# Kernel optimization log

Measured on AMD Instinct MI355X. Metric: run time of the kernel, lower is better.

## Reference

```python
import jax, jax.numpy as jnp
import numpy as np

IMG_SIZE = 640
STRIDES = (8, 16, 32)
KA = 3          # anchors per level
C = 80          # num classes
CONF_THRESH = 0.001
NMS_THRESH = 0.6
TOPK = 4096     # fixed candidate cap for jit-compatible NMS


def setup_inputs() -> dict:
    key = jax.random.key(0)
    k1, k2, k3 = jax.random.split(key, 3)
    ch = KA * (1 + C + 4)  # 255
    pred_s = jax.random.normal(k1, (ch, 80, 80), dtype=jnp.float32)
    pred_m = jax.random.normal(k2, (ch, 40, 40), dtype=jnp.float32)
    pred_l = jax.random.normal(k3, (ch, 20, 20), dtype=jnp.float32)
    # classic YOLOv3 anchors, [level, anchor, (w,h)]
    anchor_size = jnp.array(
        [[[10, 13], [16, 30], [33, 23]],
         [[30, 61], [62, 45], [59, 119]],
         [[116, 90], [156, 198], [373, 326]]], dtype=jnp.float32)
    return {"pred_s": pred_s, "pred_m": pred_m, "pred_l": pred_l,
            "anchor_size": anchor_size}


def _decode_level(pred, anchors, stride):
    # pred: [KA*(1+C+4), H, W]; anchors: [KA, 2]
    H, W = pred.shape[1], pred.shape[2]
    p = jnp.transpose(pred, (1, 2, 0))                    # [H, W, ch]
    obj = p[..., :KA].reshape(-1, 1)                      # [H*W*KA, 1]
    cls = p[..., KA:KA * (1 + C)].reshape(-1, C)          # [H*W*KA, C]
    reg = p[..., KA * (1 + C):].reshape(H * W, KA, 4)     # [H*W, KA, 4]
    gy, gx = jnp.meshgrid(jnp.arange(H), jnp.arange(W), indexing="ij")
    grid = jnp.stack([gx, gy], -1).reshape(-1, 1, 2).astype(pred.dtype)  # [H*W,1,2]
    # center_sample = False branch
    xy = (jax.nn.sigmoid(reg[..., :2]) + grid) * stride
    wh = jnp.exp(reg[..., 2:]) * anchors[None, :, :]
    box = jnp.concatenate([xy - 0.5 * wh, xy + 0.5 * wh], -1).reshape(-1, 4)
    return obj, cls, box


def _decode(pred_s, pred_m, pred_l, anchor_size):
    parts = [_decode_level(p, anchor_size[i], STRIDES[i])
             for i, p in enumerate([pred_s, pred_m, pred_l])]
    obj = jnp.concatenate([p[0] for p in parts], 0)       # [N,1]
    cls = jnp.concatenate([p[1] for p in parts], 0)       # [N,C]
    box = jnp.concatenate([p[2] for p in parts], 0)       # [N,4]
    bboxes = jnp.clip(box / IMG_SIZE, 0.0, 1.0)
    scores = jax.nn.sigmoid(obj) * jax.nn.softmax(cls, axis=-1)
    return bboxes, scores


def reference(pred_s, pred_m, pred_l, anchor_size):
    bboxes, scores = _decode(pred_s, pred_m, pred_l, anchor_size)
    cls_inds = jnp.argmax(scores, axis=1)                 # [N]
    sc = jnp.max(scores, axis=1)                          # [N]
    sc_masked = jnp.where(sc >= CONF_THRESH, sc, -1.0)
    top_sc, idx = jax.lax.top_k(sc_masked, TOPK)          # candidates, score-sorted
    b = bboxes[idx]                                       # [K,4]
    c = cls_inds[idx]                                     # [K]
    valid = top_sc >= CONF_THRESH                         # [K]
    # pairwise IoU, exactly as the numpy NMS computes it
    x1, y1, x2, y2 = b[:, 0], b[:, 1], b[:, 2], b[:, 3]
    area = (x2 - x1) * (y2 - y1)
    xx1 = jnp.maximum(x1[:, None], x1[None, :])
    yy1 = jnp.maximum(y1[:, None], y1[None, :])
    xx2 = jnp.minimum(x2[:, None], x2[None, :])
    yy2 = jnp.minimum(y2[:, None], y2[None, :])
    w = jnp.maximum(1e-28, xx2 - xx1)
    h = jnp.maximum(1e-28, yy2 - yy1)
    inter = w * h
    iou = inter / (area[:, None] + area[None, :] - inter + 1e-14)
    # sup[j, i] = kept j (earlier in score order) suppresses i, same class only
    order = jnp.arange(TOPK)
    sup = (c[:, None] == c[None, :]) & (iou > NMS_THRESH) \
          & (order[:, None] < order[None, :])
    def body(i, keep):
        ki = valid[i] & ~jnp.any(keep & sup[:, i])
        return keep.at[i].set(ki)
    keep = jax.lax.fori_loop(0, TOPK, body, jnp.zeros(TOPK, dtype=bool))
    return b, top_sc, c, keep
```

## Files before the change

### kernel.cpp

```cpp
#include <hip/hip_runtime.h>
#include <cstdint>
#include <cstddef>

#define N_ANCH 25200
#define NB0 19200
#define NB1 24000
#define TOPK_N 4096
#define CONF_T 0.001
#define NMS_T 0.6
#define IMGS 640.0
#define NBINS 8192
#define JS 16

typedef unsigned long long u64;

struct WS {
  alignas(64) double sc[N_ANCH];
  alignas(64) double box[N_ANCH][4];
  alignas(64) int    cls[N_ANCH];
  alignas(64) int    binv[N_ANCH];
  alignas(64) int    rank[N_ANCH];
  alignas(64) int    subset[N_ANCH];
  alignas(64) double ssc[N_ANCH];
  int    m_count;
  int    t_bin;
  alignas(64) double tbox[TOPK_N][4];
  alignas(64) double tarea[TOPK_N];
  alignas(64) double tsc[TOPK_N];
  alignas(64) int    tcls[TOPK_N];
  alignas(64) u64    supT[TOPK_N * 64];
  alignas(64) u64    hasSup[64];
};

__device__ __forceinline__ double dsigmoid(double x) { return 1.0 / (1.0 + exp(-x)); }

__device__ __forceinline__ int score_bin(double sc) {
  if (sc < 0.0) return 0;
  return (int)(__float_as_uint((float)sc) >> 17);
}

__global__ void k_decode(const float* __restrict__ ps, const float* __restrict__ pm,
                         const float* __restrict__ pl, const float* __restrict__ anch,
                         WS* __restrict__ ws) {
  int tid = blockIdx.x * 256 + threadIdx.x;
  int a = tid >> 2;
  int r = tid & 3;
  if (a >= N_ANCH) return;
  const float* p; int W, base, lvl; double stride;
  if (a < NB0)      { p = ps; W = 80; base = 0;   lvl = 0; stride = 8.0; }
  else if (a < NB1) { p = pm; W = 40; base = NB0; lvl = 1; stride = 16.0; }
  else              { p = pl; W = 20; base = NB1; lvl = 2; stride = 32.0; }
  int e = a - base;
  int pos = e / 3;
  int k = e - 3 * pos;
  int HW = W * W;

  const float* pc = p + (size_t)(3 + k * 80) * HW + pos;
  double m = -1e300, ssum = 0.0; int am = 0;
  for (int t = 0; t < 20; ++t) {
    int c = r + 4 * t;
    double v = (double)pc[(size_t)c * HW];
    ssum += exp(v);
    if (v > m) { m = v; am = c; }
  }
  for (int off = 1; off <= 2; off <<= 1) {
    double om = __shfl_xor(m, off);
    int oam   = __shfl_xor(am, off);
    double os = __shfl_xor(ssum, off);
    ssum += os;
    if (om > m || (om == m && oam < am)) { m = om; am = oam; }
  }

  if (r == 0) {
    double sobj = dsigmoid((double)p[(size_t)k * HW + pos]);
    double sc = sobj * (exp(m) / ssum);

    int x = pos % W, y = pos / W;
    const float* pr = p + (size_t)(243 + k * 4) * HW + pos;
    double tx = (double)pr[0];
    double ty = (double)pr[(size_t)HW];
    double tw = (double)pr[(size_t)2 * HW];
    double th = (double)pr[(size_t)3 * HW];
    double cx = (dsigmoid(tx) + (double)x) * stride;
    double cy = (dsigmoid(ty) + (double)y) * stride;
    double aw = (double)anch[lvl * 6 + k * 2 + 0];
    double ah = (double)anch[lvl * 6 + k * 2 + 1];
    double bw = exp(tw) * aw;
    double bh = exp(th) * ah;
    double x1 = fmin(fmax((cx - 0.5 * bw) / IMGS, 0.0), 1.0);
    double y1 = fmin(fmax((cy - 0.5 * bh) / IMGS, 0.0), 1.0);
    double x2 = fmin(fmax((cx + 0.5 * bw) / IMGS, 0.0), 1.0);
    double y2 = fmin(fmax((cy + 0.5 * bh) / IMGS, 0.0), 1.0);

    ws->box[a][0] = x1; ws->box[a][1] = y1;
    ws->box[a][2] = x2; ws->box[a][3] = y2;
    ws->cls[a] = am;
    double scm = (sc >= CONF_T) ? sc : -1.0;
    ws->sc[a] = scm;
    ws->binv[a] = score_bin(scm);
  }
}

__global__ void __launch_bounds__(1024) k_select(WS* __restrict__ ws) {
  __shared__ int hist[NBINS];
  __shared__ int part[1024];
  int t = threadIdx.x;
  for (int i = t; i < NBINS; i += 1024) hist[i] = 0;
  __syncthreads();
  for (int i = t; i < N_ANCH; i += 1024) atomicAdd(&hist[ws->binv[i]], 1);
  __syncthreads();
  const int CH = NBINS / 1024;
  int sum = 0;
  for (int rr = 0; rr < CH; ++rr) sum += hist[NBINS - 1 - (t * CH + rr)];
  part[t] = sum;
  __syncthreads();
  for (int off = 1; off < 1024; off <<= 1) {
    int v = (t >= off) ? part[t - off] : 0;
    __syncthreads();
    part[t] += v;
    __syncthreads();
  }
  int cum = part[t] - sum;
  for (int rr = 0; rr < CH; ++rr) {
    int b = NBINS - 1 - (t * CH + rr);
    int h = hist[b];
    int prev = cum;
    cum += h;
    if (prev < TOPK_N && cum >= TOPK_N) ws->t_bin = b;
  }
  if (t == 0) ws->m_count = 0;
}

__global__ void k_compact(WS* __restrict__ ws) {
  int i = blockIdx.x * 256 + threadIdx.x;
  if (i < 64) ws->hasSup[i] = 0ull;
  if (i >= N_ANCH) return;
  int tb = ws->t_bin;
  if (ws->binv[i] >= tb) {
    int idx = atomicAdd(&ws->m_count, 1);
    ws->subset[idx] = i;
    ws->ssc[idx] = ws->sc[i];
    ws->rank[idx] = 0;
  }
}

__global__ void k_rank(WS* __restrict__ ws) {
  const int CHUNK = 1024;
  __shared__ double sj[CHUNK];
  __shared__ int    aj[CHUNK];
  int m = ws->m_count;
  if ((int)blockIdx.x * 256 >= m) return;
  int i = blockIdx.x * 256 + threadIdx.x;
  bool active = (i < m);
  int ai = active ? ws->subset[i] : 0;
  double si = active ? ws->ssc[i] : -2.0;

  int jlen = (m + JS - 1) / JS;
  int j0 = blockIdx.y * jlen;
  int jend = min(j0 + jlen, m);
  int cnt = 0;
  for (int jc = j0; jc < jend; jc += CHUNK) {
    int n = min(CHUNK, jend - jc);
    __syncthreads();
    for (int t = threadIdx.x; t < n; t += 256) {
      aj[t] = ws->subset[jc + t];
      sj[t] = ws->ssc[jc + t];
    }
    __syncthreads();
    if (active) {
      for (int t = 0; t < n; ++t) {
        double s = sj[t];
        cnt += (int)((s > si) | ((s == si) & (aj[t] < ai)));
      }
    }
  }
  if (active && cnt) atomicAdd(&ws->rank[i], cnt);
}

__global__ void k_scatter(WS* __restrict__ ws, float* __restrict__ out) {
  int m = ws->m_count;
  int i = blockIdx.x * 256 + threadIdx.x;
  if (i >= m) return;
  int r = ws->rank[i];
  if (r >= TOPK_N) return;
  int a = ws->subset[i];
  double b0 = ws->box[a][0], b1 = ws->box[a][1];
  double b2 = ws->box[a][2], b3 = ws->box[a][3];
  double s  = ws->ssc[i];
  int    c  = ws->cls[a];
  ws->tbox[r][0] = b0; ws->tbox[r][1] = b1;
  ws->tbox[r][2] = b2; ws->tbox[r][3] = b3;
  ws->tarea[r] = (b2 - b0) * (b3 - b1);
  ws->tsc[r] = s;
  ws->tcls[r] = c;
  out[r * 4 + 0] = (float)b0;
  out[r * 4 + 1] = (float)b1;
  out[r * 4 + 2] = (float)b2;
  out[r * 4 + 3] = (float)b3;
  out[4 * TOPK_N + r] = (float)s;
  out[5 * TOPK_N + r] = (float)c;
}

__global__ void k_iou(WS* __restrict__ ws) {
  int tid = threadIdx.x;
  int w = blockIdx.y;
  int i0 = blockIdx.x * 256;
  int jbase = w * 64;
  if (jbase >= i0 + 256) {
    ws->supT[(size_t)(i0 + tid) * 64 + w] = 0ull;
    return;
  }
  __shared__ double jb[64][5];
  __shared__ int jc[64];
  if (tid < 64) {
    int j = jbase + tid;
    jb[tid][0] = ws->tbox[j][0];
    jb[tid][1] = ws->tbox[j][1];
    jb[tid][2] = ws->tbox[j][2];
    jb[tid][3] = ws->tbox[j][3];
    jb[tid][4] = ws->tarea[j];
    jc[tid] = ws->tcls[j];
  }
  __syncthreads();
  int i = i0 + tid;
  double x1 = ws->tbox[i][0], y1 = ws->tbox[i][1];
  double x2 = ws->tbox[i][2], y2 = ws->tbox[i][3];
  double ai = ws->tarea[i];
  int ci = ws->tcls[i];
  u64 bits = 0;
  for (int t = 0; t < 64; ++t) {
    double xx1 = fmax(x1, jb[t][0]);
    double yy1 = fmax(y1, jb[t][1]);
    double xx2 = fmin(x2, jb[t][2]);
    double yy2 = fmin(y2, jb[t][3]);
    double iw = fmax(1e-28, xx2 - xx1);
    double ih = fmax(1e-28, yy2 - yy1);
    double inter = iw * ih;
    double denom = ai + jb[t][4] - inter + 1e-14;
    bool sup = (jc[t] == ci) && (inter > NMS_T * denom) && ((jbase + t) < i);
    bits |= ((u64)sup) << t;
  }
  ws->supT[(size_t)i * 64 + w] = bits;
  if (bits) atomicOr(&ws->hasSup[i >> 6], 1ull << (i & 63));
}

__global__ void __launch_bounds__(64) k_nms(const WS* __restrict__ ws, float* __restrict__ out) {
  __shared__ u64 hsArr[64];
  __shared__ int lst[TOPK_N];
  int lane = threadIdx.x;

  u64 validw = 0;
  const double4* tp = (const double4*)(ws->tsc + lane * 64);
  for (int q = 0; q < 16; ++q) {
    double4 v = tp[q];
    validw |= ((u64)(v.x >= CONF_T)) << (q * 4 + 0);
    validw |= ((u64)(v.y >= CONF_T)) << (q * 4 + 1);
    validw |= ((u64)(v.z >= CONF_T)) << (q * 4 + 2);
    validw |= ((u64)(v.w >= CONF_T)) << (q * 4 + 3);
  }

  u64 hasw = ws->hasSup[lane];
  u64 keepw = validw & ~hasw;
  hsArr[lane] = hasw;
  __syncthreads();

  int K = 0;
  for (int l = 0; l < 64; ++l) {
    u64 w = hsArr[l];
    while (w) {
      int b = __builtin_ctzll(w);
      w &= w - 1;
      if (lane == 0) lst[K] = l * 64 + b;
      ++K;
    }
  }
  __syncthreads();

  const u64* ST = ws->supT;
  int IA[16], IB[16];
  u64 A[16], B[16];

#pragma unroll
  for (int r = 0; r < 16; ++r) IA[r] = (r < K) ? lst[r] : 0;
#pragma unroll
  for (int r = 0; r < 16; ++r) A[r] = (r < K) ? ST[(size_t)IA[r] * 64 + lane] : 0ull;

  for (int base = 0; base < K; base += 32) {
#pragma unroll
    for (int r = 0; r < 16; ++r) IB[r] = (base + 16 + r < K) ? lst[base + 16 + r] : 0;
#pragma unroll
    for (int r = 0; r < 16; ++r) B[r] = (base + 16 + r < K) ? ST[(size_t)IB[r] * 64 + lane] : 0ull;
#pragma unroll
    for (int r = 0; r < 16; ++r) {
      if (base + r < K) {
        int i = IA[r];
        u64 bal = __ballot((keepw & A[r]) != 0ull);
        if (lane == (i >> 6) && bal == 0ull && ((validw >> (i & 63)) & 1ull))
          keepw |= 1ull << (i & 63);
      }
    }
#pragma unroll
    for (int r = 0; r < 16; ++r) IA[r] = (base + 32 + r < K) ? lst[base + 32 + r] : 0;
#pragma unroll
    for (int r = 0; r < 16; ++r) A[r] = (base + 32 + r < K) ? ST[(size_t)IA[r] * 64 + lane] : 0ull;
#pragma unroll
    for (int r = 0; r < 16; ++r) {
      if (base + 16 + r < K) {
        int i = IB[r];
        u64 bal = __ballot((keepw & B[r]) != 0ull);
        if (lane == (i >> 6) && bal == 0ull && ((validw >> (i & 63)) & 1ull))
          keepw |= 1ull << (i & 63);
      }
    }
  }

  for (int b = 0; b < 64; ++b)
    out[6 * TOPK_N + lane * 64 + b] = (float)((keepw >> b) & 1ull);
}

extern "C" void kernel_launch(void* const* d_in, const int* in_sizes, int n_in,
                              void* d_out, int out_size, void* d_ws, size_t ws_size,
                              hipStream_t stream) {
  const float* ps   = (const float*)d_in[0];
  const float* pm   = (const float*)d_in[1];
  const float* pl   = (const float*)d_in[2];
  const float* anch = (const float*)d_in[3];
  float* out = (float*)d_out;
  WS* ws = (WS*)d_ws;

  dim3 blk(256);
  k_decode <<<dim3((N_ANCH * 4 + 255) / 256), blk, 0, stream>>>(ps, pm, pl, anch, ws);
  k_select <<<dim3(1), dim3(1024), 0, stream>>>(ws);
  k_compact<<<dim3((N_ANCH + 255) / 256), blk, 0, stream>>>(ws);
  k_rank   <<<dim3((N_ANCH + 255) / 256, JS), blk, 0, stream>>>(ws);
  k_scatter<<<dim3((N_ANCH + 255) / 256), blk, 0, stream>>>(ws, out);
  k_iou    <<<dim3(TOPK_N / 256, 64), blk, 0, stream>>>(ws);
  k_nms    <<<dim3(1), dim3(64), 0, stream>>>(ws, out);
}
```

Measured before the change: 124.1 us.

## Fuse all NMS pipeline stages into one cooperative kernel with grid syncs

The seven separate launches (decode, select, compact, rank, scatter, IoU, NMS) are replaced by one cooperative kernel of 256 blocks × 512 threads, with grid.sync between stages. This removes per-launch overhead and gaps between kernels. The score histogram is now built with global atomics during decode instead of in a single-block pass. Compaction uses wave-aggregated atomics, and rank and IoU work is spread over persistent blocks through task loops. In exchange it adds grid-wide barrier costs, global-atomic contention on the histogram, and leaves most of the grid idle during the single-block select and NMS stages.

```diff
diff --git a/kernel.cpp b/kernel.cpp
--- a/kernel.cpp
+++ b/kernel.cpp
@@ -1,6 +1,9 @@
 #include <hip/hip_runtime.h>
+#include <hip/hip_cooperative_groups.h>
 #include <cstdint>
 #include <cstddef>
+
+namespace cg = cooperative_groups;
 
 #define N_ANCH 25200
 #define NB0 19200
@@ -10,7 +13,9 @@
 #define NMS_T 0.6
 #define IMGS 640.0
 #define NBINS 8192
-#define JS 16
+#define JS 32
+#define NBLK 256
+#define NTHR 512
 
 typedef unsigned long long u64;
 
@@ -22,6 +27,8 @@
   alignas(64) int    rank[N_ANCH];
   alignas(64) int    subset[N_ANCH];
   alignas(64) double ssc[N_ANCH];
+  alignas(64) int    hist[NBINS];
+  alignas(64) u64    hasSup[64];
   int    m_count;
   int    t_bin;
   alignas(64) double tbox[TOPK_N][4];
@@ -29,7 +36,6 @@
   alignas(64) double tsc[TOPK_N];
   alignas(64) int    tcls[TOPK_N];
   alignas(64) u64    supT[TOPK_N * 64];
-  alignas(64) u64    hasSup[64];
 };
 
 __device__ __forceinline__ double dsigmoid(double x) { return 1.0 / (1.0 + exp(-x)); }
@@ -39,283 +45,323 @@
   return (int)(__float_as_uint((float)sc) >> 17);
 }
 
-__global__ void k_decode(const float* __restrict__ ps, const float* __restrict__ pm,
-                         const float* __restrict__ pl, const float* __restrict__ anch,
-                         WS* __restrict__ ws) {
-  int tid = blockIdx.x * 256 + threadIdx.x;
-  int a = tid >> 2;
-  int r = tid & 3;
-  if (a >= N_ANCH) return;
-  const float* p; int W, base, lvl; double stride;
-  if (a < NB0)      { p = ps; W = 80; base = 0;   lvl = 0; stride = 8.0; }
-  else if (a < NB1) { p = pm; W = 40; base = NB0; lvl = 1; stride = 16.0; }
-  else              { p = pl; W = 20; base = NB1; lvl = 2; stride = 32.0; }
-  int e = a - base;
-  int pos = e / 3;
-  int k = e - 3 * pos;
-  int HW = W * W;
-
-  const float* pc = p + (size_t)(3 + k * 80) * HW + pos;
-  double m = -1e300, ssum = 0.0; int am = 0;
-  for (int t = 0; t < 20; ++t) {
-    int c = r + 4 * t;
-    double v = (double)pc[(size_t)c * HW];
-    ssum += exp(v);
-    if (v > m) { m = v; am = c; }
-  }
-  for (int off = 1; off <= 2; off <<= 1) {
-    double om = __shfl_xor(m, off);
-    int oam   = __shfl_xor(am, off);
-    double os = __shfl_xor(ssum, off);
-    ssum += os;
-    if (om > m || (om == m && oam < am)) { m = om; am = oam; }
-  }
-
-  if (r == 0) {
-    double sobj = dsigmoid((double)p[(size_t)k * HW + pos]);
-    double sc = sobj * (exp(m) / ssum);
-
-    int x = pos % W, y = pos / W;
-    const float* pr = p + (size_t)(243 + k * 4) * HW + pos;
-    double tx = (double)pr[0];
-    double ty = (double)pr[(size_t)HW];
-    double tw = (double)pr[(size_t)2 * HW];
-    double th = (double)pr[(size_t)3 * HW];
-    double cx = (dsigmoid(tx) + (double)x) * stride;
-    double cy = (dsigmoid(ty) + (double)y) * stride;
-    double aw = (double)anch[lvl * 6 + k * 2 + 0];
-    double ah = (double)anch[lvl * 6 + k * 2 + 1];
-    double bw = exp(tw) * aw;
-    double bh = exp(th) * ah;
-    double x1 = fmin(fmax((cx - 0.5 * bw) / IMGS, 0.0), 1.0);
-    double y1 = fmin(fmax((cy - 0.5 * bh) / IMGS, 0.0), 1.0);
-    double x2 = fmin(fmax((cx + 0.5 * bw) / IMGS, 0.0), 1.0);
-    double y2 = fmin(fmax((cy + 0.5 * bh) / IMGS, 0.0), 1.0);
-
-    ws->box[a][0] = x1; ws->box[a][1] = y1;
-    ws->box[a][2] = x2; ws->box[a][3] = y2;
-    ws->cls[a] = am;
-    double scm = (sc >= CONF_T) ? sc : -1.0;
-    ws->sc[a] = scm;
-    ws->binv[a] = score_bin(scm);
-  }
-}
-
-__global__ void __launch_bounds__(1024) k_select(WS* __restrict__ ws) {
-  __shared__ int hist[NBINS];
-  __shared__ int part[1024];
-  int t = threadIdx.x;
-  for (int i = t; i < NBINS; i += 1024) hist[i] = 0;
-  __syncthreads();
-  for (int i = t; i < N_ANCH; i += 1024) atomicAdd(&hist[ws->binv[i]], 1);
-  __syncthreads();
-  const int CH = NBINS / 1024;
-  int sum = 0;
-  for (int rr = 0; rr < CH; ++rr) sum += hist[NBINS - 1 - (t * CH + rr)];
-  part[t] = sum;
-  __syncthreads();
-  for (int off = 1; off < 1024; off <<= 1) {
-    int v = (t >= off) ? part[t - off] : 0;
+__global__ void __launch_bounds__(NTHR)
+k_all(const float* __restrict__ ps, const float* __restrict__ pm,
+      const float* __restrict__ pl, const float* __restrict__ anch,
+      WS* __restrict__ ws, float* __restrict__ out) {
+  cg::grid_group grid = cg::this_grid();
+  const int tid  = threadIdx.x;
+  const int bid  = blockIdx.x;
+  const int gtid = bid * NTHR + tid;
+
+  __shared__ int    part[NTHR];
+  __shared__ double sjD[NTHR];
+  __shared__ int    ajA[NTHR];
+  __shared__ double jbD[128][5];
+  __shared__ int    jcA[128];
+  __shared__ u64    hsArr[64];
+  __shared__ int    lst[TOPK_N];
+
+  if (gtid < NBINS) ws->hist[gtid] = 0;
+  else if (gtid < NBINS + 64) ws->hasSup[gtid - NBINS] = 0ull;
+  else if (gtid == NBINS + 64) ws->m_count = 0;
+  grid.sync();
+
+  {
+    int a = gtid >> 2;
+    int r = gtid & 3;
+    if (a < N_ANCH) {
+      const float* p; int W, base, lvl; double stride;
+      if (a < NB0)      { p = ps; W = 80; base = 0;   lvl = 0; stride = 8.0; }
+      else if (a < NB1) { p = pm; W = 40; base = NB0; lvl = 1; stride = 16.0; }
+      else              { p = pl; W = 20; base = NB1; lvl = 2; stride = 32.0; }
+      int e = a - base;
+      int pos = e / 3;
+      int k = e - 3 * pos;
+      int HW = W * W;
+
+      const float* pc = p + (size_t)(3 + k * 80) * HW + pos;
+      double m = -1e300, ssum = 0.0; int am = 0;
+      for (int t = 0; t < 20; ++t) {
+        int c = r + 4 * t;
+        double v = (double)pc[(size_t)c * HW];
+        ssum += exp(v);
+        if (v > m) { m = v; am = c; }
+      }
+      for (int off = 1; off <= 2; off <<= 1) {
+        double om = __shfl_xor(m, off);
+        int oam   = __shfl_xor(am, off);
+        double os = __shfl_xor(ssum, off);
+        ssum += os;
+        if (om > m || (om == m && oam < am)) { m = om; am = oam; }
+      }
+
+      if (r == 0) {
+        double sobj = dsigmoid((double)p[(size_t)k * HW + pos]);
+        double sc = sobj * (exp(m) / ssum);
+
+        int x = pos % W, y = pos / W;
+        const float* pr = p + (size_t)(243 + k * 4) * HW + pos;
+        double tx = (double)pr[0];
+        double ty = (double)pr[(size_t)HW];
+        double tw = (double)pr[(size_t)2 * HW];
+        double th = (double)pr[(size_t)3 * HW];
+        double cx = (dsigmoid(tx) + (double)x) * stride;
+        double cy = (dsigmoid(ty) + (double)y) * stride;
+        double aw = (double)anch[lvl * 6 + k * 2 + 0];
+        double ah = (double)anch[lvl * 6 + k * 2 + 1];
+        double bw = exp(tw) * aw;
+        double bh = exp(th) * ah;
+        double x1 = fmin(fmax((cx - 0.5 * bw) / IMGS, 0.0), 1.0);
+        double y1 = fmin(fmax((cy - 0.5 * bh) / IMGS, 0.0), 1.0);
+        double x2 = fmin(fmax((cx + 0.5 * bw) / IMGS, 0.0), 1.0);
+        double y2 = fmin(fmax((cy + 0.5 * bh) / IMGS, 0.0), 1.0);
+
+        ws->box[a][0] = x1; ws->box[a][1] = y1;
+        ws->box[a][2] = x2; ws->box[a][3] = y2;
+        ws->cls[a] = am;
+        double scm = (sc >= CONF_T) ? sc : -1.0;
+        ws->sc[a] = scm;
+        int bv = score_bin(scm);
+        ws->binv[a] = bv;
+        atomicAdd(&ws->hist[bv], 1);
+      }
+    }
+  }
+  grid.sync();
+
+  if (bid == 0) {
+    const int CH = NBINS / NTHR;
+    int h16[CH];
+    int sum = 0;
+#pragma unroll
+    for (int rr = 0; rr < CH; ++rr) {
+      h16[rr] = ws->hist[NBINS - 1 - (tid * CH + rr)];
+      sum += h16[rr];
+    }
+    part[tid] = sum;
     __syncthreads();
-    part[t] += v;
+    for (int off = 1; off < NTHR; off <<= 1) {
+      int v = (tid >= off) ? part[tid - off] : 0;
+      __syncthreads();
+      part[tid] += v;
+      __syncthreads();
+    }
+    int cum = part[tid] - sum;
+#pragma unroll
+    for (int rr = 0; rr < CH; ++rr) {
+      int b = NBINS - 1 - (tid * CH + rr);
+      int h = h16[rr];
+      int prev = cum;
+      cum += h;
+      if (prev < TOPK_N && cum >= TOPK_N) ws->t_bin = b;
+    }
+  }
+  grid.sync();
+
+  {
+    bool want = false;
+    if (gtid < N_ANCH) want = (ws->binv[gtid] >= ws->t_bin);
+    u64 mask = __ballot(want);
+    if (mask) {
+      int lane = tid & 63;
+      int lead = __ffsll(mask) - 1;
+      int pre  = __popcll(mask & ((1ull << lane) - 1ull));
+      int base = 0;
+      if (lane == lead) base = atomicAdd(&ws->m_count, __popcll(mask));
+      base = __shfl(base, lead);
+      if (want) {
+        int idx = base + pre;
+        ws->subset[idx] = gtid;
+        ws->ssc[idx] = ws->sc[gtid];
+        ws->rank[idx] = 0;
+      }
+    }
+  }
+  grid.sync();
+
+  {
+    int m = ws->m_count;
+    int itc = (m + NTHR - 1) / NTHR;
+    int ntask = itc * JS;
+    int jlen = (m + JS - 1) / JS;
+    for (int task = bid; task < ntask; task += NBLK) {
+      int it = task / JS, js = task % JS;
+      int i = it * NTHR + tid;
+      bool active = (i < m);
+      int ai = active ? ws->subset[i] : 0;
+      double si = active ? ws->ssc[i] : -2.0;
+      int j0 = js * jlen;
+      int jend = min(j0 + jlen, m);
+      int cnt = 0;
+      for (int jc0 = j0; jc0 < jend; jc0 += NTHR) {
+        int n = min(NTHR, jend - jc0);
+        __syncthreads();
+        if (tid < n) { ajA[tid] = ws->subset[jc0 + tid]; sjD[tid] = ws->ssc[jc0 + tid]; }
+        __syncthreads();
+        if (active) {
+          for (int t = 0; t < n; ++t) {
+            double s = sjD[t];
+            cnt += (int)((s > si) | ((s == si) & (ajA[t] < ai)));
+          }
+        }
+      }
+      if (active && cnt) atomicAdd(&ws->rank[i], cnt);
+    }
+  }
+  grid.sync();
+
+  {
+    int m = ws->m_count;
+    if (gtid < m) {
+      int r = ws->rank[gtid];
+      if (r < TOPK_N) {
+        int a = ws->subset[gtid];
+        double b0 = ws->box[a][0], b1 = ws->box[a][1];
+        double b2 = ws->box[a][2], b3 = ws->box[a][3];
+        double s  = ws->ssc[gtid];
+        int    c  = ws->cls[a];
+        ws->tbox[r][0] = b0; ws->tbox[r][1] = b1;
+        ws->tbox[r][2] = b2; ws->tbox[r][3] = b3;
+        ws->tarea[r] = (b2 - b0) * (b3 - b1);
+        ws->tsc[r] = s;
+        ws->tcls[r] = c;
+        out[r * 4 + 0] = (float)b0;
+        out[r * 4 + 1] = (float)b1;
+        out[r * 4 + 2] = (float)b2;
+        out[r * 4 + 3] = (float)b3;
+        out[4 * TOPK_N + r] = (float)s;
+        out[5 * TOPK_N + r] = (float)c;
+      }
+    }
+  }
+  grid.sync();
+
+  {
+    for (int task = bid; task < 512; task += NBLK) {
+      int biT = task >> 5, wp = task & 31;
+      int i0 = biT * 256;
+      int jb0 = wp * 128;
+      int il = tid & 255;
+      int wq = tid >> 8;
+      int w = wp * 2 + wq;
+      int jbase = w * 64;
+      int i = i0 + il;
+      if (jb0 >= i0 + 256) {
+        ws->supT[(size_t)i * 64 + w] = 0ull;
+      } else {
+        __syncthreads();
+        if (tid < 128) {
+          int j = jb0 + tid;
+          jbD[tid][0] = ws->tbox[j][0];
+          jbD[tid][1] = ws->tbox[j][1];
+          jbD[tid][2] = ws->tbox[j][2];
+          jbD[tid][3] = ws->tbox[j][3];
+          jbD[tid][4] = ws->tarea[j];
+          jcA[tid] = ws->tcls[j];
+        }
+        __syncthreads();
+        double x1 = ws->tbox[i][0], y1 = ws->tbox[i][1];
+        double x2 = ws->tbox[i][2], y2 = ws->tbox[i][3];
+        double ai = ws->tarea[i];
+        int ci = ws->tcls[i];
+        int tb = wq * 64;
+        u64 bits = 0;
+        for (int t = 0; t < 64; ++t) {
+          double xx1 = fmax(x1, jbD[tb + t][0]);
+          double yy1 = fmax(y1, jbD[tb + t][1]);
+          double xx2 = fmin(x2, jbD[tb + t][2]);
+          double yy2 = fmin(y2, jbD[tb + t][3]);
+          double iw = fmax(1e-28, xx2 - xx1);
+          double ih = fmax(1e-28, yy2 - yy1);
+          double inter = iw * ih;
+          double denom = ai + jbD[tb + t][4] - inter + 1e-14;
+          bool sup = (jcA[tb + t] == ci) && (inter > NMS_T * denom) && ((jbase + t) < i);
+          bits |= ((u64)sup) << t;
+        }
+        ws->supT[(size_t)i * 64 + w] = bits;
+        if (bits) atomicOr(&ws->hasSup[i >> 6], 1ull << (i & 63));
+      }
+    }
+  }
+  grid.sync();
+
+  if (bid == 0) {
+    bool w0 = (tid < 64);
+    int lane = tid;
+    u64 validw = 0, hasw = 0, keepw = 0;
+    if (w0) {
+      const double4* tp = (const double4*)(ws->tsc + lane * 64);
+      for (int q = 0; q < 16; ++q) {
+        double4 v = tp[q];
+        validw |= ((u64)(v.x >= CONF_T)) << (q * 4 + 0);
+        validw |= ((u64)(v.y >= CONF_T)) << (q * 4 + 1);
+        validw |= ((u64)(v.z >= CONF_T)) << (q * 4 + 2);
+        validw |= ((u64)(v.w >= CONF_T)) << (q * 4 + 3);
+      }
+      hasw = ws->hasSup[lane];
+      keepw = validw & ~hasw;
+      hsArr[lane] = hasw;
+    }
     __syncthreads();
-  }
-  int cum = part[t] - sum;
-  for (int rr = 0; rr < CH; ++rr) {
-    int b = NBINS - 1 - (t * CH + rr);
-    int h = hist[b];
-    int prev = cum;
-    cum += h;
-    if (prev < TOPK_N && cum >= TOPK_N) ws->t_bin = b;
-  }
-  if (t == 0) ws->m_count = 0;
-}
-
-__global__ void k_compact(WS* __restrict__ ws) {
-  int i = blockIdx.x * 256 + threadIdx.x;
-  if (i < 64) ws->hasSup[i] = 0ull;
-  if (i >= N_ANCH) return;
-  int tb = ws->t_bin;
-  if (ws->binv[i] >= tb) {
-    int idx = atomicAdd(&ws->m_count, 1);
-    ws->subset[idx] = i;
-    ws->ssc[idx] = ws->sc[i];
-    ws->rank[idx] = 0;
-  }
-}
-
-__global__ void k_rank(WS* __restrict__ ws) {
-  const int CHUNK = 1024;
-  __shared__ double sj[CHUNK];
-  __shared__ int    aj[CHUNK];
-  int m = ws->m_count;
-  if ((int)blockIdx.x * 256 >= m) return;
-  int i = blockIdx.x * 256 + threadIdx.x;
-  bool active = (i < m);
-  int ai = active ? ws->subset[i] : 0;
-  double si = active ? ws->ssc[i] : -2.0;
-
-  int jlen = (m + JS - 1) / JS;
-  int j0 = blockIdx.y * jlen;
-  int jend = min(j0 + jlen, m);
-  int cnt = 0;
-  for (int jc = j0; jc < jend; jc += CHUNK) {
-    int n = min(CHUNK, jend - jc);
+
+    int K = 0;
+    if (w0) {
+      for (int l = 0; l < 64; ++l) {
+        u64 wv = hsArr[l];
+        while (wv) {
+          int b = __builtin_ctzll(wv);
+          wv &= wv - 1;
+          if (lane == 0) lst[K] = l * 64 + b;
+          ++K;
+        }
+      }
+    }
     __syncthreads();
-    for (int t = threadIdx.x; t < n; t += 256) {
-      aj[t] = ws->subset[jc + t];
-      sj[t] = ws->ssc[jc + t];
-    }
-    __syncthreads();
-    if (active) {
-      for (int t = 0; t < n; ++t) {
-        double s = sj[t];
-        cnt += (int)((s > si) | ((s == si) & (aj[t] < ai)));
-      }
-    }
-  }
-  if (active && cnt) atomicAdd(&ws->rank[i], cnt);
-}
-
-__global__ void k_scatter(WS* __restrict__ ws, float* __restrict__ out) {
-  int m = ws->m_count;
-  int i = blockIdx.x * 256 + threadIdx.x;
-  if (i >= m) return;
-  int r = ws->rank[i];
-  if (r >= TOPK_N) return;
-  int a = ws->subset[i];
-  double b0 = ws->box[a][0], b1 = ws->box[a][1];
-  double b2 = ws->box[a][2], b3 = ws->box[a][3];
-  double s  = ws->ssc[i];
-  int    c  = ws->cls[a];
-  ws->tbox[r][0] = b0; ws->tbox[r][1] = b1;
-  ws->tbox[r][2] = b2; ws->tbox[r][3] = b3;
-  ws->tarea[r] = (b2 - b0) * (b3 - b1);
-  ws->tsc[r] = s;
-  ws->tcls[r] = c;
-  out[r * 4 + 0] = (float)b0;
-  out[r * 4 + 1] = (float)b1;
-  out[r * 4 + 2] = (float)b2;
-  out[r * 4 + 3] = (float)b3;
-  out[4 * TOPK_N + r] = (float)s;
-  out[5 * TOPK_N + r] = (float)c;
-}
-
-__global__ void k_iou(WS* __restrict__ ws) {
-  int tid = threadIdx.x;
-  int w = blockIdx.y;
-  int i0 = blockIdx.x * 256;
-  int jbase = w * 64;
-  if (jbase >= i0 + 256) {
-    ws->supT[(size_t)(i0 + tid) * 64 + w] = 0ull;
-    return;
-  }
-  __shared__ double jb[64][5];
-  __shared__ int jc[64];
-  if (tid < 64) {
-    int j = jbase + tid;
-    jb[tid][0] = ws->tbox[j][0];
-    jb[tid][1] = ws->tbox[j][1];
-    jb[tid][2] = ws->tbox[j][2];
-    jb[tid][3] = ws->tbox[j][3];
-    jb[tid][4] = ws->tarea[j];
-    jc[tid] = ws->tcls[j];
-  }
-  __syncthreads();
-  int i = i0 + tid;
-  double x1 = ws->tbox[i][0], y1 = ws->tbox[i][1];
-  double x2 = ws->tbox[i][2], y2 = ws->tbox[i][3];
-  double ai = ws->tarea[i];
-  int ci = ws->tcls[i];
-  u64 bits = 0;
-  for (int t = 0; t < 64; ++t) {
-    double xx1 = fmax(x1, jb[t][0]);
-    double yy1 = fmax(y1, jb[t][1]);
-    double xx2 = fmin(x2, jb[t][2]);
-    double yy2 = fmin(y2, jb[t][3]);
-    double iw = fmax(1e-28, xx2 - xx1);
-    double ih = fmax(1e-28, yy2 - yy1);
-    double inter = iw * ih;
-    double denom = ai + jb[t][4] - inter + 1e-14;
-    bool sup = (jc[t] == ci) && (inter > NMS_T * denom) && ((jbase + t) < i);
-    bits |= ((u64)sup) << t;
-  }
-  ws->supT[(size_t)i * 64 + w] = bits;
-  if (bits) atomicOr(&ws->hasSup[i >> 6], 1ull << (i & 63));
-}
-
-__global__ void __launch_bounds__(64) k_nms(const WS* __restrict__ ws, float* __restrict__ out) {
-  __shared__ u64 hsArr[64];
-  __shared__ int lst[TOPK_N];
-  int lane = threadIdx.x;
-
-  u64 validw = 0;
-  const double4* tp = (const double4*)(ws->tsc + lane * 64);
-  for (int q = 0; q < 16; ++q) {
-    double4 v = tp[q];
-    validw |= ((u64)(v.x >= CONF_T)) << (q * 4 + 0);
-    validw |= ((u64)(v.y >= CONF_T)) << (q * 4 + 1);
-    validw |= ((u64)(v.z >= CONF_T)) << (q * 4 + 2);
-    validw |= ((u64)(v.w >= CONF_T)) << (q * 4 + 3);
-  }
-
-  u64 hasw = ws->hasSup[lane];
-  u64 keepw = validw & ~hasw;
-  hsArr[lane] = hasw;
-  __syncthreads();
-
-  int K = 0;
-  for (int l = 0; l < 64; ++l) {
-    u64 w = hsArr[l];
-    while (w) {
-      int b = __builtin_ctzll(w);
-      w &= w - 1;
-      if (lane == 0) lst[K] = l * 64 + b;
-      ++K;
-    }
-  }
-  __syncthreads();
-
-  const u64* ST = ws->supT;
-  int IA[16], IB[16];
-  u64 A[16], B[16];
-
-#pragma unroll
-  for (int r = 0; r < 16; ++r) IA[r] = (r < K) ? lst[r] : 0;
-#pragma unroll
-  for (int r = 0; r < 16; ++r) A[r] = (r < K) ? ST[(size_t)IA[r] * 64 + lane] : 0ull;
-
-  for (int base = 0; base < K; base += 32) {
-#pragma unroll
-    for (int r = 0; r < 16; ++r) IB[r] = (base + 16 + r < K) ? lst[base + 16 + r] : 0;
-#pragma unroll
-    for (int r = 0; r < 16; ++r) B[r] = (base + 16 + r < K) ? ST[(size_t)IB[r] * 64 + lane] : 0ull;
-#pragma unroll
-    for (int r = 0; r < 16; ++r) {
-      if (base + r < K) {
-        int i = IA[r];
-        u64 bal = __ballot((keepw & A[r]) != 0ull);
-        if (lane == (i >> 6) && bal == 0ull && ((validw >> (i & 63)) & 1ull))
-          keepw |= 1ull << (i & 63);
-      }
-    }
-#pragma unroll
-    for (int r = 0; r < 16; ++r) IA[r] = (base + 32 + r < K) ? lst[base + 32 + r] : 0;
-#pragma unroll
-    for (int r = 0; r < 16; ++r) A[r] = (base + 32 + r < K) ? ST[(size_t)IA[r] * 64 + lane] : 0ull;
-#pragma unroll
-    for (int r = 0; r < 16; ++r) {
-      if (base + 16 + r < K) {
-        int i = IB[r];
-        u64 bal = __ballot((keepw & B[r]) != 0ull);
-        if (lane == (i >> 6) && bal == 0ull && ((validw >> (i & 63)) & 1ull))
-          keepw |= 1ull << (i & 63);
-      }
-    }
-  }
-
-  for (int b = 0; b < 64; ++b)
-    out[6 * TOPK_N + lane * 64 + b] = (float)((keepw >> b) & 1ull);
+
+    if (w0) {
+      const u64* ST = ws->supT;
+      int IA[16], IB[16];
+      u64 A[16], B[16];
+
+#pragma unroll
+      for (int r = 0; r < 16; ++r) IA[r] = (r < K) ? lst[r] : 0;
+#pragma unroll
+      for (int r = 0; r < 16; ++r) A[r] = (r < K) ? ST[(size_t)IA[r] * 64 + lane] : 0ull;
+
+      for (int base = 0; base < K; base += 32) {
+#pragma unroll
+        for (int r = 0; r < 16; ++r) IB[r] = (base + 16 + r < K) ? lst[base + 16 + r] : 0;
+#pragma unroll
+        for (int r = 0; r < 16; ++r) B[r] = (base + 16 + r < K) ? ST[(size_t)IB[r] * 64 + lane] : 0ull;
+#pragma unroll
+        for (int r = 0; r < 16; ++r) {
+          if (base + r < K) {
+            int i = IA[r];
+            u64 bal = __ballot((keepw & A[r]) != 0ull);
+            if (lane == (i >> 6) && bal == 0ull && ((validw >> (i & 63)) & 1ull))
+              keepw |= 1ull << (i & 63);
+          }
+        }
+#pragma unroll
+        for (int r = 0; r < 16; ++r) IA[r] = (base + 32 + r < K) ? lst[base + 32 + r] : 0;
+#pragma unroll
+        for (int r = 0; r < 16; ++r) A[r] = (base + 32 + r < K) ? ST[(size_t)IA[r] * 64 + lane] : 0ull;
+#pragma unroll
+        for (int r = 0; r < 16; ++r) {
+          if (base + 16 + r < K) {
+            int i = IB[r];
+            u64 bal = __ballot((keepw & B[r]) != 0ull);
+            if (lane == (i >> 6) && bal == 0ull && ((validw >> (i & 63)) & 1ull))
+              keepw |= 1ull << (i & 63);
+          }
+        }
+      }
+
+      for (int b = 0; b < 64; ++b)
+        out[6 * TOPK_N + lane * 64 + b] = (float)((keepw >> b) & 1ull);
+    }
+  }
 }
 
 extern "C" void kernel_launch(void* const* d_in, const int* in_sizes, int n_in,
@@ -328,12 +374,6 @@
   float* out = (float*)d_out;
   WS* ws = (WS*)d_ws;
 
-  dim3 blk(256);
-  k_decode <<<dim3((N_ANCH * 4 + 255) / 256), blk, 0, stream>>>(ps, pm, pl, anch, ws);
-  k_select <<<dim3(1), dim3(1024), 0, stream>>>(ws);
-  k_compact<<<dim3((N_ANCH + 255) / 256), blk, 0, stream>>>(ws);
-  k_rank   <<<dim3((N_ANCH + 255) / 256, JS), blk, 0, stream>>>(ws);
-  k_scatter<<<dim3((N_ANCH + 255) / 256), blk, 0, stream>>>(ws, out);
-  k_iou    <<<dim3(TOPK_N / 256, 64), blk, 0, stream>>>(ws);
-  k_nms    <<<dim3(1), dim3(64), 0, stream>>>(ws, out);
+  void* args[] = { (void*)&ps, (void*)&pm, (void*)&pl, (void*)&anch, (void*)&ws, (void*)&out };
+  hipLaunchCooperativeKernel((void*)k_all, dim3(NBLK), dim3(NTHR), args, 0, stream);
 }
```

Result: slower. 309.8 us (+149.6%).
